# Optimization experiments

Hardware: AMD Instinct MI355X
Metric: run time of the kernel (lower is better)

## Reference

```python
import jax, jax.numpy as jnp
import numpy as np

S = 7
STEP = 1.0 / S
LAMBDA_COORD = 5.0
LAMBDA_NOOBJ = 0.5


def setup_inputs() -> dict:
    key = jax.random.key(0)
    k1, k2, k3 = jax.random.split(key, 3)
    B = 16384
    pred = jax.random.uniform(k1, (B, S, S, 30), dtype=jnp.float32)
    target = jax.random.uniform(k2, (B, S, S, 30), dtype=jnp.float32)
    conf = (jax.random.uniform(k3, (B, S, S)) > 0.9).astype(jnp.float32)
    target = target.at[..., 4].set(conf)
    return {"pred": pred, "target": target}


def _convert_box(box):
    # box: [..., S, S, 4] in cell-relative (x, y, w, h); returns clipped corners.
    gi = jnp.arange(S, dtype=box.dtype).reshape(1, S, 1)  # first spatial axis -> x offset
    gj = jnp.arange(S, dtype=box.dtype).reshape(1, 1, S)  # second spatial axis -> y offset
    x, y, w, h = box[..., 0], box[..., 1], box[..., 2], box[..., 3]
    cx = (x + gi) * STEP
    cy = (y + gj) * STEP
    x1 = jnp.maximum(cx - w / 2, 0.0)
    y1 = jnp.maximum(cy - h / 2, 0.0)
    x2 = jnp.minimum(cx + w / 2, 1.0)
    y2 = jnp.minimum(cy + h / 2, 1.0)
    return x1, y1, x2, y2


def _iou(b1, b2):
    a, b, c, d = b1
    q, w, e, r = b2
    minx = jnp.maximum(a, q)
    miny = jnp.maximum(b, w)
    maxx = jnp.minimum(c, e)
    maxy = jnp.minimum(d, r)
    inter = (maxy - miny) * (maxx - minx)  # faithful: no clamping of negative overlaps
    union = (e - q) * (r - w) + (d - b) * (c - a) - inter
    return jnp.where(inter > 0, inter / (union + 1e-05), 0.0)


def reference(pred, target):
    B = pred.shape[0]
    tbox = _convert_box(target[..., :4])
    pbox1 = _convert_box(pred[..., 0:4])
    pbox2 = _convert_box(pred[..., 5:9])
    iou1 = _iou(tbox, pbox1)  # [B, S, S]
    iou2 = _iou(tbox, pbox2)

    sel2 = iou1 <= iou2  # original: box1 responsible only if iou1 > iou2
    conf_t = jax.lax.stop_gradient(jnp.where(sel2, iou2, iou1))  # .item() detached iou
    pxy = jnp.where(sel2[..., None], pred[..., 5:7], pred[..., 0:2])
    pwh = jnp.where(sel2[..., None], pred[..., 7:9], pred[..., 2:4])
    pconf = jnp.where(sel2, pred[..., 9], pred[..., 4])

    obj = (target[..., 4] > 0).astype(pred.dtype)  # [B, S, S]
    noobj = (target[..., 4] == 0).astype(pred.dtype)

    obj_loss = jnp.sum(obj * (pconf - conf_t) ** 2)
    xy_loss = jnp.sum(obj[..., None] * (pxy - target[..., 0:2]) ** 2)
    wh_loss = jnp.sum(obj[..., None] * (pwh - target[..., 2:4]) ** 2)
    class_loss = jnp.sum(obj[..., None] * (pred[..., 10:] - target[..., 10:]) ** 2)
    noobj_loss = jnp.sum(noobj * ((pred[..., 4] - target[..., 4]) ** 2 + (pred[..., 9] - target[..., 9]) ** 2))

    loss = obj_loss + LAMBDA_NOOBJ * noobj_loss + LAMBDA_COORD * (xy_loss + wh_loss) + class_loss
    return loss / B
```

## Files before the change

### kernel.cpp

```cpp
#include <hip/hip_runtime.h>


#define NS 7
#define NC 30
#define CPB 256
#define F4_PER_CHUNK (CPB * NC / 4)

__global__ __launch_bounds__(256) void yolo_loss_kernel(
    const float* __restrict__ pred,
    const float* __restrict__ targ,
    float* __restrict__ out, float inv_B)
{
    const float STEP = 1.0f / 7.0f;
    const float L_COORD = 5.0f;
    const float L_NOOBJ = 0.5f;

    __shared__ float sp[CPB * NC];
    __shared__ float st[CPB * NC];

    const int tid = threadIdx.x;
    const size_t base_f = (size_t)blockIdx.x * (CPB * NC);

    {
        const float4* __restrict__ gp4 = (const float4*)(pred + base_f);
        const float4* __restrict__ gt4 = (const float4*)(targ + base_f);
        float4* sp4 = (float4*)sp;
        float4* st4 = (float4*)st;
        #pragma unroll
        for (int k = tid; k < F4_PER_CHUNK; k += 256) {
            sp4[k] = gp4[k];
            st4[k] = gt4[k];
        }
    }
    __syncthreads();

    const int cell = blockIdx.x * CPB + tid;
    const int j = cell % NS;
    const int i = (cell / NS) % NS;
    const float gi = (float)i;
    const float gj = (float)j;

    float p[NC], t[NC];
    {
        const float2* lp2 = (const float2*)(sp + tid * NC);
        const float2* lt2 = (const float2*)(st + tid * NC);
        #pragma unroll
        for (int k = 0; k < NC / 2; ++k) {
            float2 v = lp2[k]; p[2 * k] = v.x; p[2 * k + 1] = v.y;
            float2 u = lt2[k]; t[2 * k] = u.x; t[2 * k + 1] = u.y;
        }
    }

    float ta, tb, tc, td;
    {
        float cx = (t[0] + gi) * STEP;
        float cy = (t[1] + gj) * STEP;
        ta = fmaxf(cx - t[2] * 0.5f, 0.0f);
        tb = fmaxf(cy - t[3] * 0.5f, 0.0f);
        tc = fminf(cx + t[2] * 0.5f, 1.0f);
        td = fminf(cy + t[3] * 0.5f, 1.0f);
    }
    float q1, w1, e1, r1;
    {
        float cx = (p[0] + gi) * STEP;
        float cy = (p[1] + gj) * STEP;
        q1 = fmaxf(cx - p[2] * 0.5f, 0.0f);
        w1 = fmaxf(cy - p[3] * 0.5f, 0.0f);
        e1 = fminf(cx + p[2] * 0.5f, 1.0f);
        r1 = fminf(cy + p[3] * 0.5f, 1.0f);
    }
    float q2, w2, e2, r2;
    {
        float cx = (p[5] + gi) * STEP;
        float cy = (p[6] + gj) * STEP;
        q2 = fmaxf(cx - p[7] * 0.5f, 0.0f);
        w2 = fmaxf(cy - p[8] * 0.5f, 0.0f);
        e2 = fminf(cx + p[7] * 0.5f, 1.0f);
        r2 = fminf(cy + p[8] * 0.5f, 1.0f);
    }

    float tarea = (td - tb) * (tc - ta);
    float iou1, iou2;
    {
        float minx = fmaxf(ta, q1), miny = fmaxf(tb, w1);
        float maxx = fminf(tc, e1), maxy = fminf(td, r1);
        float inter = (maxy - miny) * (maxx - minx);
        float uni = (e1 - q1) * (r1 - w1) + tarea - inter;
        iou1 = (inter > 0.0f) ? inter / (uni + 1e-5f) : 0.0f;
    }
    {
        float minx = fmaxf(ta, q2), miny = fmaxf(tb, w2);
        float maxx = fminf(tc, e2), maxy = fminf(td, r2);
        float inter = (maxy - miny) * (maxx - minx);
        float uni = (e2 - q2) * (r2 - w2) + tarea - inter;
        iou2 = (inter > 0.0f) ? inter / (uni + 1e-5f) : 0.0f;
    }

    bool sel2 = (iou1 <= iou2);
    float conf_t = sel2 ? iou2 : iou1;
    float px = sel2 ? p[5] : p[0];
    float py = sel2 ? p[6] : p[1];
    float pw = sel2 ? p[7] : p[2];
    float ph = sel2 ? p[8] : p[3];
    float pconf = sel2 ? p[9] : p[4];

    float obj = (t[4] > 0.0f) ? 1.0f : 0.0f;
    float noobj = (t[4] == 0.0f) ? 1.0f : 0.0f;

    float dx = px - t[0], dy = py - t[1];
    float dw = pw - t[2], dh = ph - t[3];
    float coord = dx * dx + dy * dy + dw * dw + dh * dh;

    float dc = pconf - conf_t;
    float obj_loss = dc * dc;

    float cls = 0.0f;
    #pragma unroll
    for (int k = 10; k < NC; ++k) {
        float d = p[k] - t[k];
        cls += d * d;
    }

    float d4 = p[4] - t[4];
    float d9 = p[9] - t[9];
    float noobj_loss = d4 * d4 + d9 * d9;

    float lsum = obj * (obj_loss + L_COORD * coord + cls) + L_NOOBJ * noobj * noobj_loss;

    #pragma unroll
    for (int off = 32; off > 0; off >>= 1)
        lsum += __shfl_down(lsum, off, 64);

    __shared__ float wsum[4];
    int lane = tid & 63;
    int wid = tid >> 6;
    if (lane == 0) wsum[wid] = lsum;
    __syncthreads();
    if (tid == 0) {
        float s = (wsum[0] + wsum[1]) + (wsum[2] + wsum[3]);
        atomicAdd(out, s * inv_B);
    }
}

extern "C" void kernel_launch(void* const* d_in, const int* in_sizes, int n_in,
                              void* d_out, int out_size, void* d_ws, size_t ws_size,
                              hipStream_t stream) {
    const float* pred = (const float*)d_in[0];
    const float* targ = (const float*)d_in[1];
    float* out = (float*)d_out;

    const int B = 16384;
    const int n_cells = B * NS * NS;
    const float inv_B = 1.0f / (float)B;

    hipMemsetAsync(out, 0, sizeof(float) * out_size, stream);

    const int grid = n_cells / CPB;
    yolo_loss_kernel<<<grid, 256, 0, stream>>>(pred, targ, out, inv_B);
}
```

Baseline: 209.4 us.

## Stage inputs into LDS with direct global_load_lds and halve block size

Replaces the register-staged float4 copy of pred and target into shared memory with the global_load_lds builtin, which writes global data straight into LDS without passing through VGPRs. Each of two waves loads one tensor in 15 wide 16-byte transfers. The block shrinks to 128 threads covering 128 cells, which doubles the grid and halves LDS per block so more blocks can be resident. The copy loop hard-codes 15 iterations of 1024 bytes and the wave-to-tensor mapping, so it depends on the block size staying 128 and on the 16-byte LDS-load variant being supported by the target.

```diff
diff --git a/kernel.cpp b/kernel.cpp
--- a/kernel.cpp
+++ b/kernel.cpp
@@ -3,10 +3,14 @@
 
 #define NS 7
 #define NC 30
-#define CPB 256
-#define F4_PER_CHUNK (CPB * NC / 4)
+#define CPB 128
+#define BLOCK 128
+#define CHUNK_FLOATS (CPB * NC)
 
-__global__ __launch_bounds__(256) void yolo_loss_kernel(
+typedef __attribute__((address_space(1))) const float global_float;
+typedef __attribute__((address_space(3))) float lds_float;
+
+__global__ __launch_bounds__(BLOCK) void yolo_loss_kernel(
     const float* __restrict__ pred,
     const float* __restrict__ targ,
     float* __restrict__ out, float inv_B)
@@ -15,21 +19,23 @@
     const float L_COORD = 5.0f;
     const float L_NOOBJ = 0.5f;
 
-    __shared__ float sp[CPB * NC];
-    __shared__ float st[CPB * NC];
+    __shared__ float sbuf[2 * CHUNK_FLOATS];
 
     const int tid = threadIdx.x;
-    const size_t base_f = (size_t)blockIdx.x * (CPB * NC);
+    const int wave = tid >> 6;
+    const int lane = tid & 63;
 
     {
-        const float4* __restrict__ gp4 = (const float4*)(pred + base_f);
-        const float4* __restrict__ gt4 = (const float4*)(targ + base_f);
-        float4* sp4 = (float4*)sp;
-        float4* st4 = (float4*)st;
+        const size_t base_bytes = (size_t)blockIdx.x * (CHUNK_FLOATS * 4);
+        const char* gbase = (const char*)(wave == 0 ? pred : targ) + base_bytes
+                          + (size_t)lane * 16;
+        char* lbase = (char*)sbuf + wave * (CHUNK_FLOATS * 4);
         #pragma unroll
-        for (int k = tid; k < F4_PER_CHUNK; k += 256) {
-            sp4[k] = gp4[k];
-            st4[k] = gt4[k];
+        for (int i = 0; i < 15; ++i) {
+            __builtin_amdgcn_global_load_lds(
+                (global_float*)(gbase + i * 1024),
+                (lds_float*)(lbase + i * 1024),
+                16, 0, 0);
         }
     }
     __syncthreads();
@@ -42,8 +48,8 @@
 
     float p[NC], t[NC];
     {
-        const float2* lp2 = (const float2*)(sp + tid * NC);
-        const float2* lt2 = (const float2*)(st + tid * NC);
+        const float2* lp2 = (const float2*)(sbuf + tid * NC);
+        const float2* lt2 = (const float2*)(sbuf + CHUNK_FLOATS + tid * NC);
         #pragma unroll
         for (int k = 0; k < NC / 2; ++k) {
             float2 v = lp2[k]; p[2 * k] = v.x; p[2 * k + 1] = v.y;
@@ -131,14 +137,11 @@
     for (int off = 32; off > 0; off >>= 1)
         lsum += __shfl_down(lsum, off, 64);
 
-    __shared__ float wsum[4];
-    int lane = tid & 63;
-    int wid = tid >> 6;
-    if (lane == 0) wsum[wid] = lsum;
+    __shared__ float wsum[2];
+    if (lane == 0) wsum[wave] = lsum;
     __syncthreads();
     if (tid == 0) {
-        float s = (wsum[0] + wsum[1]) + (wsum[2] + wsum[3]);
-        atomicAdd(out, s * inv_B);
+        atomicAdd(out, (wsum[0] + wsum[1]) * inv_B);
     }
 }
 
@@ -156,5 +159,5 @@
     hipMemsetAsync(out, 0, sizeof(float) * out_size, stream);
 
     const int grid = n_cells / CPB;
-    yolo_loss_kernel<<<grid, 256, 0, stream>>>(pred, targ, out, inv_B);
+    yolo_loss_kernel<<<grid, BLOCK, 0, stream>>>(pred, targ, out, inv_B);
 }
```

After: 231.0 us. +10.3%, slower.
